# Optimization experiments

Hardware: AMD Instinct MI355X
Metric: run time of the kernel (lower is better)

The kernel has to match this reference:

```python
import jax, jax.numpy as jnp
import numpy as np

Q_DIM = 1024
K_DIM = 1024
V_DIM = 1024
ATTEN_DIM = 1024
NUM_HEADS = 16
HEAD_DIM = ATTEN_DIM // NUM_HEADS
B, L = 4, 2048


def setup_inputs() -> dict:
    key = jax.random.key(0)
    ks = jax.random.split(key, 11)
    s = 0.02
    return {
        "query": jax.random.normal(ks[0], (B, L, Q_DIM), dtype=jnp.float32),
        "key":   jax.random.normal(ks[1], (B, L, K_DIM), dtype=jnp.float32),
        "value": jax.random.normal(ks[2], (B, L, V_DIM), dtype=jnp.float32),
        "Wq": jax.random.normal(ks[3], (Q_DIM, ATTEN_DIM), dtype=jnp.float32) * s,
        "bq": jnp.zeros((ATTEN_DIM,), dtype=jnp.float32),
        "Wk": jax.random.normal(ks[4], (K_DIM, ATTEN_DIM), dtype=jnp.float32) * s,
        "bk": jnp.zeros((ATTEN_DIM,), dtype=jnp.float32),
        "Wv": jax.random.normal(ks[5], (V_DIM, ATTEN_DIM), dtype=jnp.float32) * s,
        "bv": jnp.zeros((ATTEN_DIM,), dtype=jnp.float32),
        "Wo": jax.random.normal(ks[6], (ATTEN_DIM, V_DIM), dtype=jnp.float32) * s,
        "bo": jnp.zeros((V_DIM,), dtype=jnp.float32),
    }


def reference(query, key, value, Wq, bq, Wk, bk, Wv, bv, Wo, bo):
    # QKV projections
    q = query @ Wq + bq        # [B, L, A]
    k = key   @ Wk + bk        # [B, L, A]
    v = value @ Wv + bv        # [B, L, A]
    # split heads: [B, L, H, D]
    def split_heads(x):
        return x.reshape(x.shape[:-1] + (NUM_HEADS, HEAD_DIM))
    q, k, v = split_heads(q), split_heads(k), split_heads(v)
    scale = 1.0 / (HEAD_DIM ** 0.5)
    # scores: [B, H, Lq, Lk]
    scores = jnp.einsum("bqhd,bkhd->bhqk", q, k) * scale
    attn = jax.nn.softmax(scores, axis=-1)
    out = jnp.einsum("bhqk,bkhd->bqhd", attn, v)  # [B, Lq, H, D]
    out = out.reshape(out.shape[0], out.shape[1], ATTEN_DIM)
    return out @ Wo + bo
```

## Files before the change

kernel.cpp:

```cpp
#include <hip/hip_runtime.h>
#include <stdint.h>

#define L_SEQ 2048
#define BATCH 4
#define ADIM  1024
#define NH    16
#define HD    64

typedef __attribute__((ext_vector_type(8))) short bf16x8;
typedef __attribute__((ext_vector_type(4))) float f32x4;
typedef __attribute__((ext_vector_type(16))) float f32x16;
typedef __attribute__((ext_vector_type(2))) int i32x2;

__device__ __forceinline__ short f2bf(float f) {
    union { float f; unsigned u; } x; x.f = f;
    unsigned r = x.u + 0x7fffu + ((x.u >> 16) & 1u);
    return (short)(r >> 16);
}

__device__ __forceinline__ void async_ld16(void* lds, const void* g) {
    __builtin_amdgcn_global_load_lds(
        (const __attribute__((address_space(1))) void*)g,
        (__attribute__((address_space(3))) void*)lds, 16, 0, 0);
}

__device__ __forceinline__ int cvtpk_bf16(float a, float b) {
    int r;
    asm("v_cvt_pk_bf16_f32 %0, %1, %2" : "=v"(r) : "v"(a), "v"(b));
    return r;
}

__device__ __forceinline__ bf16x8 pack4(int a, int b, int c, int d) {
    union { int i[4]; bf16x8 v; } u;
    u.i[0] = a; u.i[1] = b; u.i[2] = c; u.i[3] = d;
    return u.v;
}

__global__ void cvt3_kernel(const float* __restrict__ s0, const float* __restrict__ s1,
                            const float* __restrict__ s2, short* __restrict__ dst, int n4) {
    int i = blockIdx.x * blockDim.x + threadIdx.x;
    if (i >= n4) return;
    int z = blockIdx.y;
    const float* src = (z == 0) ? s0 : (z == 1) ? s1 : s2;
    float4 v = reinterpret_cast<const float4*>(src)[i];
    short4 s;
    s.x = f2bf(v.x); s.y = f2bf(v.y); s.z = f2bf(v.z); s.w = f2bf(v.w);
    reinterpret_cast<short4*>(dst + (size_t)z * (BATCH * L_SEQ * ADIM))[i] = s;
}

__global__ void transpose4_kernel(const float* __restrict__ W0, const float* __restrict__ W1,
                                  const float* __restrict__ W2, const float* __restrict__ W3,
                                  short* __restrict__ outb) {
    __shared__ float t[32][33];
    int z = blockIdx.z;
    const float* in = (z == 0) ? W0 : (z == 1) ? W1 : (z == 2) ? W2 : W3;
    short* out = outb + (size_t)z * (ADIM * ADIM);
    int x  = blockIdx.x * 32 + threadIdx.x;
    int y0 = blockIdx.y * 32 + threadIdx.y;
#pragma unroll
    for (int j = 0; j < 4; ++j)
        t[threadIdx.y + 8 * j][threadIdx.x] = in[(y0 + 8 * j) * 1024 + x];
    __syncthreads();
    int x2 = blockIdx.y * 32 + threadIdx.x;
    int y2 = blockIdx.x * 32 + threadIdx.y;
#pragma unroll
    for (int j = 0; j < 4; ++j)
        out[(y2 + 8 * j) * 1024 + x2] = f2bf(t[threadIdx.x][threadIdx.y + 8 * j]);
}

__device__ __forceinline__ void gemm_core(const short* __restrict__ A,
                                          const short* __restrict__ BT,
                                          const float* __restrict__ bias,
                                          void* __restrict__ Cout,
                                          int mode, float scalemul,
                                          int m0, int n0) {
    const int K = 1024, N = 1024;
    __shared__ __align__(16) short smem[16384];
    int tid = threadIdx.x;
    int wave = tid >> 6, lane = tid & 63, quad = lane >> 4, l16 = lane & 15;
    int wm = wave & 1, wn = wave >> 1;
    f32x4 acc[4][4] = {};

    int row = tid >> 2, ck = tid & 3;
    const short* gA0 = A  + (size_t)(m0 + row) * K + ck * 8;
    const short* gA1 = gA0 + (size_t)64 * K;
    const short* gB0 = BT + (size_t)(n0 + row) * K + ck * 8;
    const short* gB1 = gB0 + (size_t)64 * K;
    int loA0 = tid * 8, loA1 = tid * 8 + 2048;
    int loB0 = tid * 8 + 4096, loB1 = tid * 8 + 6144;

    async_ld16(smem + loA0, gA0); async_ld16(smem + loA1, gA1);
    async_ld16(smem + loB0, gB0); async_ld16(smem + loB1, gB1);
    gA0 += 32; gA1 += 32; gB0 += 32; gB1 += 32;
    __syncthreads();

    int cur = 0;
    for (int t = 0; t < 32; ++t) {
        if (t < 31) {
            int off = (cur ^ 1) * 8192;
            async_ld16(smem + off + loA0, gA0); async_ld16(smem + off + loA1, gA1);
            async_ld16(smem + off + loB0, gB0); async_ld16(smem + off + loB1, gB1);
            gA0 += 32; gA1 += 32; gB0 += 32; gB1 += 32;
        }
        const short* Ab = smem + cur * 8192;
        const short* Bb = Ab + 4096;
        bf16x8 af[4], bfr[4];
#pragma unroll
        for (int mt = 0; mt < 4; ++mt)
            af[mt] = *(const bf16x8*)&Ab[(wm * 64 + mt * 16 + l16) * 32 + quad * 8];
#pragma unroll
        for (int nt = 0; nt < 4; ++nt)
            bfr[nt] = *(const bf16x8*)&Bb[(wn * 64 + nt * 16 + l16) * 32 + quad * 8];
#pragma unroll
        for (int mt = 0; mt < 4; ++mt)
#pragma unroll
            for (int nt = 0; nt < 4; ++nt)
                acc[mt][nt] = __builtin_amdgcn_mfma_f32_16x16x32_bf16(
                    af[mt], bfr[nt], acc[mt][nt], 0, 0, 0);
        __syncthreads();
        cur ^= 1;
    }

    if (mode == 0) {
#pragma unroll
        for (int nt = 0; nt < 4; ++nt) {
            int col = n0 + wn * 64 + nt * 16 + l16;
            float bv = bias[col];
#pragma unroll
            for (int mt = 0; mt < 4; ++mt)
#pragma unroll
                for (int r = 0; r < 4; ++r) {
                    int rw = m0 + wm * 64 + mt * 16 + quad * 4 + r;
                    ((short*)Cout)[(size_t)rw * N + col] = f2bf((acc[mt][nt][r] + bv) * scalemul);
                }
        }
    } else if (mode == 1) {
        short* tw = smem + wave * 1120;
        int rbase = m0 + wm * 64;
        int bidx = rbase >> 11, lk0 = rbase & 2047;
#pragma unroll
        for (int nt = 0; nt < 4; ++nt) {
            int col0 = n0 + wn * 64 + nt * 16;
            int h = col0 >> 6, d0 = col0 & 63;
            float bv = bias[col0 + l16];
#pragma unroll
            for (int mt = 0; mt < 4; ++mt) {
                int a0 = cvtpk_bf16(acc[mt][nt][0] + bv, acc[mt][nt][1] + bv);
                int a1 = cvtpk_bf16(acc[mt][nt][2] + bv, acc[mt][nt][3] + bv);
                *(int*)&tw[l16 * 70 + mt * 16 + quad * 4]     = a0;
                *(int*)&tw[l16 * 70 + mt * 16 + quad * 4 + 2] = a1;
            }
            int dl = lane >> 2;
            short* dst = (short*)Cout +
                (((size_t)bidx * NH + h) * HD + d0 + dl) * L_SEQ + lk0;
#pragma unroll
            for (int p = 0; p < 2; ++p) {
                int ch = (lane & 3) + p * 4;
                *(bf16x8*)&dst[ch * 8] = *(const bf16x8*)&tw[dl * 70 + ch * 8];
            }
        }
    } else {
#pragma unroll
        for (int nt = 0; nt < 4; ++nt) {
            int col = n0 + wn * 64 + nt * 16 + l16;
            float bv = bias[col];
#pragma unroll
            for (int mt = 0; mt < 4; ++mt)
#pragma unroll
                for (int r = 0; r < 4; ++r) {
                    int rw = m0 + wm * 64 + mt * 16 + quad * 4 + r;
                    ((float*)Cout)[(size_t)rw * N + col] = acc[mt][nt][r] + bv;
                }
        }
    }
}

__device__ __forceinline__ void gemm_swz(int& m0, int& n0) {
    int bid = blockIdx.y * 8 + blockIdx.x;
    int swz = (bid & 7) * 64 + (bid >> 3);
    n0 = (swz & 7) * 128;
    m0 = (swz >> 3) * 128;
}

__global__ __launch_bounds__(256, 4)
void gemm_one(const short* __restrict__ A, const short* __restrict__ BT,
              const float* __restrict__ bias, void* __restrict__ Cout,
              int mode, float scalemul) {
    int m0, n0; gemm_swz(m0, n0);
    gemm_core(A, BT, bias, Cout, mode, scalemul, m0, n0);
}

__global__ __launch_bounds__(256, 4)
void qkv_gemm(const short* __restrict__ Xbase, const short* __restrict__ WTbase,
              const float* __restrict__ bq, const float* __restrict__ bk,
              const float* __restrict__ bv,
              short* __restrict__ Qb, short* __restrict__ Kb, short* __restrict__ VTout,
              float qscale) {
    int z = blockIdx.z;
    const short* A  = Xbase + (size_t)z * (BATCH * L_SEQ * ADIM);
    const short* BT = WTbase + (size_t)z * (ADIM * ADIM);
    const float* bias = (z == 0) ? bq : (z == 1) ? bk : bv;
    void* out = (z == 0) ? (void*)Qb : (z == 1) ? (void*)Kb : (void*)VTout;
    int mode = (z == 2) ? 1 : 0;
    float sm = (z == 0) ? qscale : 1.0f;
    int m0, n0; gemm_swz(m0, n0);
    gemm_core(A, BT, bias, out, mode, sm, m0, n0);
}

__global__ __launch_bounds__(256, 4)
void attn_kernel(const short* __restrict__ Qb, const short* __restrict__ Kb,
                 const short* __restrict__ VT, short* __restrict__ Oout) {
    __shared__ __align__(16) short lds[16384];
    int tid = threadIdx.x;
    int wave = tid >> 6, lane = tid & 63;
    int r31 = lane & 31, hi = lane >> 5;

    int f = (blockIdx.z * NH + blockIdx.y) * (L_SEQ / 128) + blockIdx.x;
    int swz = (f & 7) * 128 + (f >> 3);
    int qb = swz & 15;
    int h  = (swz >> 4) & 15;
    int b  = swz >> 8;

    size_t qrow = (size_t)(b * L_SEQ + qb * 128 + wave * 32 + r31) * ADIM + h * HD;
    bf16x8 qf[4];
#pragma unroll
    for (int dc = 0; dc < 4; ++dc)
        qf[dc] = *(const bf16x8*)&Qb[qrow + dc * 16 + hi * 8];

    const short* Kbase = Kb + (size_t)b * L_SEQ * ADIM + h * HD;
    const short* Vbase = VT + ((size_t)(b * NH + h) * HD) * L_SEQ;
    const short* gp[4]; int step[4]; int ldso[4];
#pragma unroll
    for (int s = 0; s < 4; ++s) {
        int j = s * 256 + tid;
        ldso[s] = j * 8;
        if (j < 512) {
            int c = j >> 6, k = j & 63;
            gp[s] = Kbase + (size_t)k * ADIM + c * 8;
            step[s] = 64 * ADIM;
        } else {
            int jv = j - 512;
            int c = jv >> 6, d = jv & 63;
            gp[s] = Vbase + (size_t)d * L_SEQ + c * 8;
            step[s] = 64;
        }
    }

    f32x16 o0 = {}, o1 = {}, lacc = {};
    const bf16x8 ones = pack4(0x3F803F80, 0x3F803F80, 0x3F803F80, 0x3F803F80);

#pragma unroll
    for (int s = 0; s < 4; ++s) { async_ld16(lds + ldso[s], gp[s]); gp[s] += step[s]; }
    __syncthreads();

    int cur = 0;
    for (int t = 0; t < 32; ++t) {
        const short* kb_l = lds + cur * 8192;
        const short* vb_l = kb_l + 4096;
        if (t < 31) {
            short* dst = lds + (cur ^ 1) * 8192;
#pragma unroll
            for (int s = 0; s < 4; ++s) { async_ld16(dst + ldso[s], gp[s]); gp[s] += step[s]; }
        }
#pragma unroll
        for (int kt = 0; kt < 2; ++kt) {
            f32x16 sv = {};
            __builtin_amdgcn_s_setprio(1);
#pragma unroll
            for (int dc = 0; dc < 4; ++dc) {
                bf16x8 kf = *(const bf16x8*)&kb_l[(((dc << 1) + hi) * 64 + kt * 32 + r31) * 8];
                sv = __builtin_amdgcn_mfma_f32_32x32x16_bf16(kf, qf[dc], sv, 0, 0, 0);
            }
            __builtin_amdgcn_s_setprio(0);
#pragma unroll
            for (int r = 0; r < 16; ++r) sv[r] = __builtin_amdgcn_exp2f(sv[r]);

            int p0 = cvtpk_bf16(sv[0],  sv[1]);
            int p1 = cvtpk_bf16(sv[2],  sv[3]);
            int p2 = cvtpk_bf16(sv[4],  sv[5]);
            int p3 = cvtpk_bf16(sv[6],  sv[7]);
            int p4 = cvtpk_bf16(sv[8],  sv[9]);
            int p5 = cvtpk_bf16(sv[10], sv[11]);
            int p6 = cvtpk_bf16(sv[12], sv[13]);
            int p7 = cvtpk_bf16(sv[14], sv[15]);
            asm volatile("v_permlane32_swap_b32 %0, %1" : "+v"(p0), "+v"(p2));
            asm volatile("v_permlane32_swap_b32 %0, %1" : "+v"(p1), "+v"(p3));
            asm volatile("v_permlane32_swap_b32 %0, %1" : "+v"(p4), "+v"(p6));
            asm volatile("v_permlane32_swap_b32 %0, %1" : "+v"(p5), "+v"(p7));
            bf16x8 pf0 = pack4(p0, p1, p2, p3);
            bf16x8 pf1 = pack4(p4, p5, p6, p7);

            bf16x8 vf00 = *(const bf16x8*)&vb_l[((kt * 4 + hi)     * 64 + r31) * 8];
            bf16x8 vf01 = *(const bf16x8*)&vb_l[((kt * 4 + 2 + hi) * 64 + r31) * 8];
            bf16x8 vf10 = *(const bf16x8*)&vb_l[((kt * 4 + hi)     * 64 + 32 + r31) * 8];
            bf16x8 vf11 = *(const bf16x8*)&vb_l[((kt * 4 + 2 + hi) * 64 + 32 + r31) * 8];
            __builtin_amdgcn_s_setprio(1);
            o0 = __builtin_amdgcn_mfma_f32_32x32x16_bf16(vf00, pf0, o0, 0, 0, 0);
            o1 = __builtin_amdgcn_mfma_f32_32x32x16_bf16(vf10, pf0, o1, 0, 0, 0);
            lacc = __builtin_amdgcn_mfma_f32_32x32x16_bf16(ones, pf0, lacc, 0, 0, 0);
            o0 = __builtin_amdgcn_mfma_f32_32x32x16_bf16(vf01, pf1, o0, 0, 0, 0);
            o1 = __builtin_amdgcn_mfma_f32_32x32x16_bf16(vf11, pf1, o1, 0, 0, 0);
            lacc = __builtin_amdgcn_mfma_f32_32x32x16_bf16(ones, pf1, lacc, 0, 0, 0);
            __builtin_amdgcn_s_setprio(0);
        }
        __syncthreads();
        cur ^= 1;
    }

    float inv = __builtin_amdgcn_rcpf(lacc[0]);

    short* tile = lds + wave * (32 * 68);
#pragma unroll
    for (int dt = 0; dt < 2; ++dt)
#pragma unroll
        for (int g = 0; g < 4; ++g) {
            int d0 = dt * 32 + g * 8 + hi * 4;
            int pa, pb;
            if (dt == 0) {
                pa = cvtpk_bf16(o0[g * 4 + 0] * inv, o0[g * 4 + 1] * inv);
                pb = cvtpk_bf16(o0[g * 4 + 2] * inv, o0[g * 4 + 3] * inv);
            } else {
                pa = cvtpk_bf16(o1[g * 4 + 0] * inv, o1[g * 4 + 1] * inv);
                pb = cvtpk_bf16(o1[g * 4 + 2] * inv, o1[g * 4 + 3] * inv);
            }
            *(i32x2*)&tile[r31 * 68 + d0] = (i32x2){pa, pb};
        }
    __syncthreads();
    size_t obase = (size_t)(b * L_SEQ + qb * 128 + wave * 32) * ADIM + h * HD;
    int rr = lane >> 3, cc = lane & 7;
#pragma unroll
    for (int p = 0; p < 4; ++p) {
        int row = p * 8 + rr;
        bf16x8 v = *(const bf16x8*)&tile[row * 68 + cc * 8];
        *(bf16x8*)&Oout[obase + (size_t)row * ADIM + cc * 8] = v;
    }
}

extern "C" void kernel_launch(void* const* d_in, const int* in_sizes, int n_in,
                              void* d_out, int out_size, void* d_ws, size_t ws_size,
                              hipStream_t stream) {
    const float* query = (const float*)d_in[0];
    const float* keyp  = (const float*)d_in[1];
    const float* value = (const float*)d_in[2];
    const float* Wq = (const float*)d_in[3];
    const float* bq = (const float*)d_in[4];
    const float* Wk = (const float*)d_in[5];
    const float* bk = (const float*)d_in[6];
    const float* Wv = (const float*)d_in[7];
    const float* bv = (const float*)d_in[8];
    const float* Wo = (const float*)d_in[9];
    const float* bo = (const float*)d_in[10];

    const float QSCALE = 0.125f * 1.44269504f;
    const size_t MB = 1ull << 20;
    const int n4 = (BATCH * L_SEQ * ADIM) / 4;
    char* w = (char*)d_ws;
    dim3 tblk(32, 8);
    dim3 gemm_grid(ADIM / 128, (BATCH * L_SEQ) / 128);
    dim3 attn_grid(L_SEQ / 128, NH, BATCH);

    if (ws_size >= 104 * MB) {
        short* X0  = (short*)(w);
        short* WT  = (short*)(w + 48 * MB);
        short* VT  = (short*)(w + 56 * MB);
        short* Kb  = (short*)(w + 72 * MB);
        short* Qb  = (short*)(w + 88 * MB);
        short* AO  = X0;

        cvt3_kernel<<<dim3(n4 / 256, 3), 256, 0, stream>>>(query, keyp, value, X0, n4);
        transpose4_kernel<<<dim3(32, 32, 4), tblk, 0, stream>>>(Wq, Wk, Wv, Wo, WT);
        qkv_gemm<<<dim3(ADIM / 128, (BATCH * L_SEQ) / 128, 3), 256, 0, stream>>>(
            X0, WT, bq, bk, bv, Qb, Kb, VT, QSCALE);
        attn_kernel<<<attn_grid, 256, 0, stream>>>(Qb, Kb, VT, AO);
        gemm_one<<<gemm_grid, 256, 0, stream>>>(AO, WT + (size_t)3 * ADIM * ADIM, bo,
                                                d_out, 2, 1.0f);
    } else {
        short* X0  = (short*)(w);
        short* WT  = (short*)(w + 16 * MB);
        short* VT  = (short*)(w + 24 * MB);
        short* Kb  = (short*)(w + 40 * MB);
        short* Qb  = (short*)(w + 56 * MB);

        transpose4_kernel<<<dim3(32, 32, 4), tblk, 0, stream>>>(Wq, Wk, Wv, Wo, WT);
        cvt3_kernel<<<dim3(n4 / 256, 1), 256, 0, stream>>>(query, query, query, X0, n4);
        gemm_one<<<gemm_grid, 256, 0, stream>>>(X0, WT, bq, Qb, 0, QSCALE);
        cvt3_kernel<<<dim3(n4 / 256, 1), 256, 0, stream>>>(keyp, keyp, keyp, X0, n4);
        gemm_one<<<gemm_grid, 256, 0, stream>>>(X0, WT + (size_t)ADIM * ADIM, bk, Kb, 0, 1.0f);
        cvt3_kernel<<<dim3(n4 / 256, 1), 256, 0, stream>>>(value, value, value, X0, n4);
        gemm_one<<<gemm_grid, 256, 0, stream>>>(X0, WT + (size_t)2 * ADIM * ADIM, bv, VT, 1, 1.0f);
        attn_kernel<<<attn_grid, 256, 0, stream>>>(Qb, Kb, VT, X0);
        gemm_one<<<gemm_grid, 256, 0, stream>>>(X0, WT + (size_t)3 * ADIM * ADIM, bo,
                                                d_out, 2, 1.0f);
    }
}
```

Baseline: 335.2 us.

## Fuse fp32-to-bf16 input conversion into QKV GEMM A-tile loads

Drops the separate cvt3 pass that turned the query, key and value activations into bf16 in workspace. A new GEMM core async-loads fp32 A tiles straight into LDS with an XOR swizzle and converts them to bf16 at fragment-load time, just before the MFMAs. This avoids writing and re-reading 48MB of bf16 activations. In exchange the A tile in LDS doubles in size, LDS use grows to 48KB and occupancy drops to 3 blocks. The conversion work is now repeated by every N-tile block, 8 times per A tile, and the small-workspace branch is removed.

Measured after the change: 352.0 us. 5.0% more time.

```diff
diff --git a/kernel.cpp b/kernel.cpp
--- a/kernel.cpp
+++ b/kernel.cpp
@@ -34,18 +34,6 @@
     union { int i[4]; bf16x8 v; } u;
     u.i[0] = a; u.i[1] = b; u.i[2] = c; u.i[3] = d;
     return u.v;
-}
-
-__global__ void cvt3_kernel(const float* __restrict__ s0, const float* __restrict__ s1,
-                            const float* __restrict__ s2, short* __restrict__ dst, int n4) {
-    int i = blockIdx.x * blockDim.x + threadIdx.x;
-    if (i >= n4) return;
-    int z = blockIdx.y;
-    const float* src = (z == 0) ? s0 : (z == 1) ? s1 : s2;
-    float4 v = reinterpret_cast<const float4*>(src)[i];
-    short4 s;
-    s.x = f2bf(v.x); s.y = f2bf(v.y); s.z = f2bf(v.z); s.w = f2bf(v.w);
-    reinterpret_cast<short4*>(dst + (size_t)z * (BATCH * L_SEQ * ADIM))[i] = s;
 }
 
 __global__ void transpose4_kernel(const float* __restrict__ W0, const float* __restrict__ W1,
@@ -66,6 +54,13 @@
 #pragma unroll
     for (int j = 0; j < 4; ++j)
         out[(y2 + 8 * j) * 1024 + x2] = f2bf(t[threadIdx.x][threadIdx.y + 8 * j]);
+}
+
+__device__ __forceinline__ void gemm_swz(int& m0, int& n0) {
+    int bid = blockIdx.y * 8 + blockIdx.x;
+    int swz = (bid & 7) * 64 + (bid >> 3);
+    n0 = (swz & 7) * 128;
+    m0 = (swz >> 3) * 128;
 }
 
 __device__ __forceinline__ void gemm_core(const short* __restrict__ A,
@@ -134,7 +129,113 @@
                     ((short*)Cout)[(size_t)rw * N + col] = f2bf((acc[mt][nt][r] + bv) * scalemul);
                 }
         }
-    } else if (mode == 1) {
+    } else {
+#pragma unroll
+        for (int nt = 0; nt < 4; ++nt) {
+            int col = n0 + wn * 64 + nt * 16 + l16;
+            float bv = bias[col];
+#pragma unroll
+            for (int mt = 0; mt < 4; ++mt)
+#pragma unroll
+                for (int r = 0; r < 4; ++r) {
+                    int rw = m0 + wm * 64 + mt * 16 + quad * 4 + r;
+                    ((float*)Cout)[(size_t)rw * N + col] = acc[mt][nt][r] + bv;
+                }
+        }
+    }
+}
+
+__global__ __launch_bounds__(256, 4)
+void gemm_one(const short* __restrict__ A, const short* __restrict__ BT,
+              const float* __restrict__ bias, void* __restrict__ Cout,
+              int mode, float scalemul) {
+    int m0, n0; gemm_swz(m0, n0);
+    gemm_core(A, BT, bias, Cout, mode, scalemul, m0, n0);
+}
+
+__device__ __forceinline__ void gemmf32_core(const float* __restrict__ A,
+                                             const short* __restrict__ BT,
+                                             const float* __restrict__ bias,
+                                             void* __restrict__ Cout,
+                                             int mode, float scalemul,
+                                             int m0, int n0) {
+    const int K = 1024, N = 1024;
+    __shared__ __align__(16) short smem[24576];
+    int tid = threadIdx.x;
+    int wave = tid >> 6, lane = tid & 63, quad = lane >> 4, l16 = lane & 15;
+    int wm = wave & 1, wn = wave >> 1;
+    f32x4 acc[4][4] = {};
+
+    const float* gA[4]; int loA[4];
+#pragma unroll
+    for (int s = 0; s < 4; ++s) {
+        int j = s * 256 + tid;
+        int row = j >> 3, c = (j & 7) ^ (row & 7);
+        gA[s] = A + (size_t)(m0 + row) * K + c * 4;
+        loA[s] = j * 8;
+    }
+    const short* gB[2]; int loB[2];
+#pragma unroll
+    for (int s = 0; s < 2; ++s) {
+        int j = s * 256 + tid;
+        int row = j >> 2, ck = j & 3;
+        gB[s] = BT + (size_t)(n0 + row) * K + ck * 8;
+        loB[s] = 8192 + j * 8;
+    }
+
+#pragma unroll
+    for (int s = 0; s < 4; ++s) { async_ld16(smem + loA[s], gA[s]); gA[s] += 32; }
+#pragma unroll
+    for (int s = 0; s < 2; ++s) { async_ld16(smem + loB[s], gB[s]); gB[s] += 32; }
+    __syncthreads();
+
+    int cur = 0;
+    for (int t = 0; t < 32; ++t) {
+        if (t < 31) {
+            int off = (cur ^ 1) * 12288;
+#pragma unroll
+            for (int s = 0; s < 4; ++s) { async_ld16(smem + off + loA[s], gA[s]); gA[s] += 32; }
+#pragma unroll
+            for (int s = 0; s < 2; ++s) { async_ld16(smem + off + loB[s], gB[s]); gB[s] += 32; }
+        }
+        const short* Ab = smem + cur * 12288;
+        const short* Bb = Ab + 8192;
+        bf16x8 af[4], bfr[4];
+#pragma unroll
+        for (int mt = 0; mt < 4; ++mt) {
+            int r = wm * 64 + mt * 16 + l16;
+            float4 f0 = *(const float4*)&Ab[(r * 8 + ((2 * quad)     ^ (r & 7))) * 8];
+            float4 f1 = *(const float4*)&Ab[(r * 8 + ((2 * quad + 1) ^ (r & 7))) * 8];
+            af[mt] = pack4(cvtpk_bf16(f0.x, f0.y), cvtpk_bf16(f0.z, f0.w),
+                           cvtpk_bf16(f1.x, f1.y), cvtpk_bf16(f1.z, f1.w));
+        }
+#pragma unroll
+        for (int nt = 0; nt < 4; ++nt)
+            bfr[nt] = *(const bf16x8*)&Bb[(wn * 64 + nt * 16 + l16) * 32 + quad * 8];
+#pragma unroll
+        for (int mt = 0; mt < 4; ++mt)
+#pragma unroll
+            for (int nt = 0; nt < 4; ++nt)
+                acc[mt][nt] = __builtin_amdgcn_mfma_f32_16x16x32_bf16(
+                    af[mt], bfr[nt], acc[mt][nt], 0, 0, 0);
+        __syncthreads();
+        cur ^= 1;
+    }
+
+    if (mode == 0) {
+#pragma unroll
+        for (int nt = 0; nt < 4; ++nt) {
+            int col = n0 + wn * 64 + nt * 16 + l16;
+            float bv = bias[col];
+#pragma unroll
+            for (int mt = 0; mt < 4; ++mt)
+#pragma unroll
+                for (int r = 0; r < 4; ++r) {
+                    int rw = m0 + wm * 64 + mt * 16 + quad * 4 + r;
+                    ((short*)Cout)[(size_t)rw * N + col] = f2bf((acc[mt][nt][r] + bv) * scalemul);
+                }
+        }
+    } else {
         short* tw = smem + wave * 1120;
         int rbase = m0 + wm * 64;
         int bidx = rbase >> 11, lk0 = rbase & 2047;
@@ -159,52 +260,25 @@
                 *(bf16x8*)&dst[ch * 8] = *(const bf16x8*)&tw[dl * 70 + ch * 8];
             }
         }
-    } else {
-#pragma unroll
-        for (int nt = 0; nt < 4; ++nt) {
-            int col = n0 + wn * 64 + nt * 16 + l16;
-            float bv = bias[col];
-#pragma unroll
-            for (int mt = 0; mt < 4; ++mt)
-#pragma unroll
-                for (int r = 0; r < 4; ++r) {
-                    int rw = m0 + wm * 64 + mt * 16 + quad * 4 + r;
-                    ((float*)Cout)[(size_t)rw * N + col] = acc[mt][nt][r] + bv;
-                }
-        }
-    }
-}
-
-__device__ __forceinline__ void gemm_swz(int& m0, int& n0) {
-    int bid = blockIdx.y * 8 + blockIdx.x;
-    int swz = (bid & 7) * 64 + (bid >> 3);
-    n0 = (swz & 7) * 128;
-    m0 = (swz >> 3) * 128;
-}
-
-__global__ __launch_bounds__(256, 4)
-void gemm_one(const short* __restrict__ A, const short* __restrict__ BT,
-              const float* __restrict__ bias, void* __restrict__ Cout,
-              int mode, float scalemul) {
-    int m0, n0; gemm_swz(m0, n0);
-    gemm_core(A, BT, bias, Cout, mode, scalemul, m0, n0);
-}
-
-__global__ __launch_bounds__(256, 4)
-void qkv_gemm(const short* __restrict__ Xbase, const short* __restrict__ WTbase,
+    }
+}
+
+__global__ __launch_bounds__(256, 3)
+void qkv_gemm(const float* __restrict__ Xq, const float* __restrict__ Xk,
+              const float* __restrict__ Xv, const short* __restrict__ WTbase,
               const float* __restrict__ bq, const float* __restrict__ bk,
               const float* __restrict__ bv,
               short* __restrict__ Qb, short* __restrict__ Kb, short* __restrict__ VTout,
               float qscale) {
     int z = blockIdx.z;
-    const short* A  = Xbase + (size_t)z * (BATCH * L_SEQ * ADIM);
+    const float* A = (z == 0) ? Xq : (z == 1) ? Xk : Xv;
     const short* BT = WTbase + (size_t)z * (ADIM * ADIM);
     const float* bias = (z == 0) ? bq : (z == 1) ? bk : bv;
     void* out = (z == 0) ? (void*)Qb : (z == 1) ? (void*)Kb : (void*)VTout;
     int mode = (z == 2) ? 1 : 0;
     float sm = (z == 0) ? qscale : 1.0f;
     int m0, n0; gemm_swz(m0, n0);
-    gemm_core(A, BT, bias, out, mode, sm, m0, n0);
+    gemmf32_core(A, BT, bias, out, mode, sm, m0, n0);
 }
 
 __global__ __launch_bounds__(256, 4)
@@ -353,43 +427,21 @@
 
     const float QSCALE = 0.125f * 1.44269504f;
     const size_t MB = 1ull << 20;
-    const int n4 = (BATCH * L_SEQ * ADIM) / 4;
     char* w = (char*)d_ws;
     dim3 tblk(32, 8);
     dim3 gemm_grid(ADIM / 128, (BATCH * L_SEQ) / 128);
     dim3 attn_grid(L_SEQ / 128, NH, BATCH);
 
-    if (ws_size >= 104 * MB) {
-        short* X0  = (short*)(w);
-        short* WT  = (short*)(w + 48 * MB);
-        short* VT  = (short*)(w + 56 * MB);
-        short* Kb  = (short*)(w + 72 * MB);
-        short* Qb  = (short*)(w + 88 * MB);
-        short* AO  = X0;
-
-        cvt3_kernel<<<dim3(n4 / 256, 3), 256, 0, stream>>>(query, keyp, value, X0, n4);
-        transpose4_kernel<<<dim3(32, 32, 4), tblk, 0, stream>>>(Wq, Wk, Wv, Wo, WT);
-        qkv_gemm<<<dim3(ADIM / 128, (BATCH * L_SEQ) / 128, 3), 256, 0, stream>>>(
-            X0, WT, bq, bk, bv, Qb, Kb, VT, QSCALE);
-        attn_kernel<<<attn_grid, 256, 0, stream>>>(Qb, Kb, VT, AO);
-        gemm_one<<<gemm_grid, 256, 0, stream>>>(AO, WT + (size_t)3 * ADIM * ADIM, bo,
-                                                d_out, 2, 1.0f);
-    } else {
-        short* X0  = (short*)(w);
-        short* WT  = (short*)(w + 16 * MB);
-        short* VT  = (short*)(w + 24 * MB);
-        short* Kb  = (short*)(w + 40 * MB);
-        short* Qb  = (short*)(w + 56 * MB);
-
-        transpose4_kernel<<<dim3(32, 32, 4), tblk, 0, stream>>>(Wq, Wk, Wv, Wo, WT);
-        cvt3_kernel<<<dim3(n4 / 256, 1), 256, 0, stream>>>(query, query, query, X0, n4);
-        gemm_one<<<gemm_grid, 256, 0, stream>>>(X0, WT, bq, Qb, 0, QSCALE);
-        cvt3_kernel<<<dim3(n4 / 256, 1), 256, 0, stream>>>(keyp, keyp, keyp, X0, n4);
-        gemm_one<<<gemm_grid, 256, 0, stream>>>(X0, WT + (size_t)ADIM * ADIM, bk, Kb, 0, 1.0f);
-        cvt3_kernel<<<dim3(n4 / 256, 1), 256, 0, stream>>>(value, value, value, X0, n4);
-        gemm_one<<<gemm_grid, 256, 0, stream>>>(X0, WT + (size_t)2 * ADIM * ADIM, bv, VT, 1, 1.0f);
-        attn_kernel<<<attn_grid, 256, 0, stream>>>(Qb, Kb, VT, X0);
-        gemm_one<<<gemm_grid, 256, 0, stream>>>(X0, WT + (size_t)3 * ADIM * ADIM, bo,
-                                                d_out, 2, 1.0f);
-    }
-}
+    short* AO = (short*)(w);
+    short* WT = (short*)(w + 16 * MB);
+    short* VT = (short*)(w + 24 * MB);
+    short* Kb = (short*)(w + 40 * MB);
+    short* Qb = (short*)(w + 56 * MB);
+
+    transpose4_kernel<<<dim3(32, 32, 4), tblk, 0, stream>>>(Wq, Wk, Wv, Wo, WT);
+    qkv_gemm<<<dim3(ADIM / 128, (BATCH * L_SEQ) / 128, 3), 256, 0, stream>>>(
+        query, keyp, value, WT, bq, bk, bv, Qb, Kb, VT, QSCALE);
+    attn_kernel<<<attn_grid, 256, 0, stream>>>(Qb, Kb, VT, AO);
+    gemm_one<<<gemm_grid, 256, 0, stream>>>(AO, WT + (size_t)3 * ADIM * ADIM, bo,
+                                            d_out, 2, 1.0f);
+}
```

## Rework GEMM into 8-wave 128x256 tiles with 4-stage ping-pong pipeline

Applied to the files above, without the earlier changes.

The projection GEMM core goes from 256-thread 128x128 tiles with a double buffer to 512-thread blocks on 128x256 tiles. It adds a four-stage LDS ring loaded asynchronously, with explicit vmcnt waits and raw s_barrier calls. MFMA work is split into half-steps interleaved with staged loads, and s_setprio raises priority during the MFMA bursts. The goal is to hide global-load latency and cut per-tile sync and reload overhead. The cost is 96KB of LDS per block, which limits occupancy, and fragile hand-tuned waitcnt ordering.

Result: no change. 330.0 us (-1.6%).

```diff
diff --git a/kernel.cpp b/kernel.cpp
--- a/kernel.cpp
+++ b/kernel.cpp
@@ -68,58 +68,100 @@
         out[(y2 + 8 * j) * 1024 + x2] = f2bf(t[threadIdx.x][threadIdx.y + 8 * j]);
 }
 
-__device__ __forceinline__ void gemm_core(const short* __restrict__ A,
-                                          const short* __restrict__ BT,
-                                          const float* __restrict__ bias,
-                                          void* __restrict__ Cout,
-                                          int mode, float scalemul,
-                                          int m0, int n0) {
+
+#define GBAR() asm volatile("s_barrier" ::: "memory")
+
+#define GP_PAIR(HB, SHB, DOSTAGE, NWAIT)                                          \
+  {                                                                               \
+    const short* Ah = smem + (HB) * 12288;                                        \
+    const short* Bh = Ah + 4096;                                                  \
+    if (DOSTAGE) {                                                                \
+      async_ld16(smem + (SHB) * 12288 + loA,  pA);                                \
+      async_ld16(smem + (SHB) * 12288 + loB0, pB0);                               \
+    }                                                                             \
+    bf16x8 b0 = *(const bf16x8*)&Bh[(wn * 64 +  0 + l16) * 32 + quad * 8];        \
+    bf16x8 b1 = *(const bf16x8*)&Bh[(wn * 64 + 16 + l16) * 32 + quad * 8];        \
+    bf16x8 b2 = *(const bf16x8*)&Bh[(wn * 64 + 32 + l16) * 32 + quad * 8];        \
+    bf16x8 b3 = *(const bf16x8*)&Bh[(wn * 64 + 48 + l16) * 32 + quad * 8];        \
+    bf16x8 a0 = *(const bf16x8*)&Ah[(wm * 64 +  0 + l16) * 32 + quad * 8];        \
+    bf16x8 a1 = *(const bf16x8*)&Ah[(wm * 64 + 16 + l16) * 32 + quad * 8];        \
+    GBAR();                                                                       \
+    __builtin_amdgcn_s_setprio(1);                                                \
+    acc[0][0] = __builtin_amdgcn_mfma_f32_16x16x32_bf16(a0, b0, acc[0][0], 0,0,0);\
+    acc[0][1] = __builtin_amdgcn_mfma_f32_16x16x32_bf16(a0, b1, acc[0][1], 0,0,0);\
+    acc[0][2] = __builtin_amdgcn_mfma_f32_16x16x32_bf16(a0, b2, acc[0][2], 0,0,0);\
+    acc[0][3] = __builtin_amdgcn_mfma_f32_16x16x32_bf16(a0, b3, acc[0][3], 0,0,0);\
+    acc[1][0] = __builtin_amdgcn_mfma_f32_16x16x32_bf16(a1, b0, acc[1][0], 0,0,0);\
+    acc[1][1] = __builtin_amdgcn_mfma_f32_16x16x32_bf16(a1, b1, acc[1][1], 0,0,0);\
+    acc[1][2] = __builtin_amdgcn_mfma_f32_16x16x32_bf16(a1, b2, acc[1][2], 0,0,0);\
+    acc[1][3] = __builtin_amdgcn_mfma_f32_16x16x32_bf16(a1, b3, acc[1][3], 0,0,0);\
+    __builtin_amdgcn_s_setprio(0);                                                \
+    GBAR();                                                                       \
+    if (DOSTAGE) {                                                                \
+      async_ld16(smem + (SHB) * 12288 + loB1, pB1);                               \
+      pA += 32; pB0 += 32; pB1 += 32;                                             \
+    }                                                                             \
+    bf16x8 a2 = *(const bf16x8*)&Ah[(wm * 64 + 32 + l16) * 32 + quad * 8];        \
+    bf16x8 a3 = *(const bf16x8*)&Ah[(wm * 64 + 48 + l16) * 32 + quad * 8];        \
+    GBAR();                                                                       \
+    __builtin_amdgcn_s_setprio(1);                                                \
+    acc[2][0] = __builtin_amdgcn_mfma_f32_16x16x32_bf16(a2, b0, acc[2][0], 0,0,0);\
+    acc[2][1] = __builtin_amdgcn_mfma_f32_16x16x32_bf16(a2, b1, acc[2][1], 0,0,0);\
+    acc[2][2] = __builtin_amdgcn_mfma_f32_16x16x32_bf16(a2, b2, acc[2][2], 0,0,0);\
+    acc[2][3] = __builtin_amdgcn_mfma_f32_16x16x32_bf16(a2, b3, acc[2][3], 0,0,0);\
+    acc[3][0] = __builtin_amdgcn_mfma_f32_16x16x32_bf16(a3, b0, acc[3][0], 0,0,0);\
+    acc[3][1] = __builtin_amdgcn_mfma_f32_16x16x32_bf16(a3, b1, acc[3][1], 0,0,0);\
+    acc[3][2] = __builtin_amdgcn_mfma_f32_16x16x32_bf16(a3, b2, acc[3][2], 0,0,0);\
+    acc[3][3] = __builtin_amdgcn_mfma_f32_16x16x32_bf16(a3, b3, acc[3][3], 0,0,0);\
+    __builtin_amdgcn_s_setprio(0);                                                \
+    if ((NWAIT) == 6)      asm volatile("s_waitcnt vmcnt(6)" ::: "memory");       \
+    else if ((NWAIT) == 3) asm volatile("s_waitcnt vmcnt(3)" ::: "memory");       \
+    else if ((NWAIT) == 0) asm volatile("s_waitcnt vmcnt(0)" ::: "memory");       \
+    __builtin_amdgcn_sched_barrier(0);                                            \
+    GBAR();                                                                       \
+  }
+
+__device__ __forceinline__ void gemm8p_core(const short* __restrict__ A,
+                                            const short* __restrict__ BT,
+                                            const float* __restrict__ bias,
+                                            void* __restrict__ Cout,
+                                            int mode, float scalemul,
+                                            int m0, int n0) {
     const int K = 1024, N = 1024;
-    __shared__ __align__(16) short smem[16384];
+    __shared__ __align__(16) short smem[49152];
     int tid = threadIdx.x;
     int wave = tid >> 6, lane = tid & 63, quad = lane >> 4, l16 = lane & 15;
-    int wm = wave & 1, wn = wave >> 1;
+    int wm = wave >> 2, wn = wave & 3;
     f32x4 acc[4][4] = {};
 
-    int row = tid >> 2, ck = tid & 3;
-    const short* gA0 = A  + (size_t)(m0 + row) * K + ck * 8;
-    const short* gA1 = gA0 + (size_t)64 * K;
-    const short* gB0 = BT + (size_t)(n0 + row) * K + ck * 8;
-    const short* gB1 = gB0 + (size_t)64 * K;
-    int loA0 = tid * 8, loA1 = tid * 8 + 2048;
-    int loB0 = tid * 8 + 4096, loB1 = tid * 8 + 6144;
-
-    async_ld16(smem + loA0, gA0); async_ld16(smem + loA1, gA1);
-    async_ld16(smem + loB0, gB0); async_ld16(smem + loB1, gB1);
-    gA0 += 32; gA1 += 32; gB0 += 32; gB1 += 32;
+    int row4 = tid >> 2, kq = tid & 3;
+    const short* pA  = A  + (size_t)(m0 + row4) * K + kq * 8;
+    const short* pB0 = BT + (size_t)(n0 + row4) * K + kq * 8;
+    const short* pB1 = BT + (size_t)(n0 + 128 + row4) * K + kq * 8;
+    int loA = tid * 8, loB0 = 4096 + tid * 8, loB1 = 8192 + tid * 8;
+
+#pragma unroll
+    for (int h = 0; h < 3; ++h) {
+        async_ld16(smem + h * 12288 + loA,  pA);
+        async_ld16(smem + h * 12288 + loB0, pB0);
+        async_ld16(smem + h * 12288 + loB1, pB1);
+        pA += 32; pB0 += 32; pB1 += 32;
+    }
+    asm volatile("s_waitcnt vmcnt(6)" ::: "memory");
+    __builtin_amdgcn_sched_barrier(0);
+    GBAR();
+
+    for (int tt = 0; tt < 7; ++tt) {
+        GP_PAIR(0, 3, true, 6)
+        GP_PAIR(1, 0, true, 6)
+        GP_PAIR(2, 1, true, 6)
+        GP_PAIR(3, 2, true, 6)
+    }
+    GP_PAIR(0, 3, true,  6)
+    GP_PAIR(1, 0, false, 3)
+    GP_PAIR(2, 1, false, 0)
+    GP_PAIR(3, 2, false, -1)
     __syncthreads();
-
-    int cur = 0;
-    for (int t = 0; t < 32; ++t) {
-        if (t < 31) {
-            int off = (cur ^ 1) * 8192;
-            async_ld16(smem + off + loA0, gA0); async_ld16(smem + off + loA1, gA1);
-            async_ld16(smem + off + loB0, gB0); async_ld16(smem + off + loB1, gB1);
-            gA0 += 32; gA1 += 32; gB0 += 32; gB1 += 32;
-        }
-        const short* Ab = smem + cur * 8192;
-        const short* Bb = Ab + 4096;
-        bf16x8 af[4], bfr[4];
-#pragma unroll
-        for (int mt = 0; mt < 4; ++mt)
-            af[mt] = *(const bf16x8*)&Ab[(wm * 64 + mt * 16 + l16) * 32 + quad * 8];
-#pragma unroll
-        for (int nt = 0; nt < 4; ++nt)
-            bfr[nt] = *(const bf16x8*)&Bb[(wn * 64 + nt * 16 + l16) * 32 + quad * 8];
-#pragma unroll
-        for (int mt = 0; mt < 4; ++mt)
-#pragma unroll
-            for (int nt = 0; nt < 4; ++nt)
-                acc[mt][nt] = __builtin_amdgcn_mfma_f32_16x16x32_bf16(
-                    af[mt], bfr[nt], acc[mt][nt], 0, 0, 0);
-        __syncthreads();
-        cur ^= 1;
-    }
 
     if (mode == 0) {
 #pragma unroll
@@ -175,22 +217,22 @@
     }
 }
 
-__device__ __forceinline__ void gemm_swz(int& m0, int& n0) {
-    int bid = blockIdx.y * 8 + blockIdx.x;
-    int swz = (bid & 7) * 64 + (bid >> 3);
-    n0 = (swz & 7) * 128;
-    m0 = (swz >> 3) * 128;
-}
-
-__global__ __launch_bounds__(256, 4)
+__device__ __forceinline__ void gemm8p_swz(int& m0, int& n0) {
+    int bid = blockIdx.y * 4 + blockIdx.x;
+    int swz = (bid & 7) * 32 + (bid >> 3);
+    n0 = (swz & 3) * 256;
+    m0 = (swz >> 2) * 128;
+}
+
+__global__ __launch_bounds__(512, 2)
 void gemm_one(const short* __restrict__ A, const short* __restrict__ BT,
               const float* __restrict__ bias, void* __restrict__ Cout,
               int mode, float scalemul) {
-    int m0, n0; gemm_swz(m0, n0);
-    gemm_core(A, BT, bias, Cout, mode, scalemul, m0, n0);
-}
-
-__global__ __launch_bounds__(256, 4)
+    int m0, n0; gemm8p_swz(m0, n0);
+    gemm8p_core(A, BT, bias, Cout, mode, scalemul, m0, n0);
+}
+
+__global__ __launch_bounds__(512, 2)
 void qkv_gemm(const short* __restrict__ Xbase, const short* __restrict__ WTbase,
               const float* __restrict__ bq, const float* __restrict__ bk,
               const float* __restrict__ bv,
@@ -203,8 +245,8 @@
     void* out = (z == 0) ? (void*)Qb : (z == 1) ? (void*)Kb : (void*)VTout;
     int mode = (z == 2) ? 1 : 0;
     float sm = (z == 0) ? qscale : 1.0f;
-    int m0, n0; gemm_swz(m0, n0);
-    gemm_core(A, BT, bias, out, mode, sm, m0, n0);
+    int m0, n0; gemm8p_swz(m0, n0);
+    gemm8p_core(A, BT, bias, out, mode, sm, m0, n0);
 }
 
 __global__ __launch_bounds__(256, 4)
@@ -356,7 +398,7 @@
     const int n4 = (BATCH * L_SEQ * ADIM) / 4;
     char* w = (char*)d_ws;
     dim3 tblk(32, 8);
-    dim3 gemm_grid(ADIM / 128, (BATCH * L_SEQ) / 128);
+    dim3 gemm_grid(ADIM / 256, (BATCH * L_SEQ) / 128);
     dim3 attn_grid(L_SEQ / 128, NH, BATCH);
 
     if (ws_size >= 104 * MB) {
@@ -369,10 +411,10 @@
 
         cvt3_kernel<<<dim3(n4 / 256, 3), 256, 0, stream>>>(query, keyp, value, X0, n4);
         transpose4_kernel<<<dim3(32, 32, 4), tblk, 0, stream>>>(Wq, Wk, Wv, Wo, WT);
-        qkv_gemm<<<dim3(ADIM / 128, (BATCH * L_SEQ) / 128, 3), 256, 0, stream>>>(
+        qkv_gemm<<<dim3(ADIM / 256, (BATCH * L_SEQ) / 128, 3), 512, 0, stream>>>(
             X0, WT, bq, bk, bv, Qb, Kb, VT, QSCALE);
         attn_kernel<<<attn_grid, 256, 0, stream>>>(Qb, Kb, VT, AO);
-        gemm_one<<<gemm_grid, 256, 0, stream>>>(AO, WT + (size_t)3 * ADIM * ADIM, bo,
+        gemm_one<<<gemm_grid, 512, 0, stream>>>(AO, WT + (size_t)3 * ADIM * ADIM, bo,
                                                 d_out, 2, 1.0f);
     } else {
         short* X0  = (short*)(w);
@@ -383,13 +425,13 @@
 
         transpose4_kernel<<<dim3(32, 32, 4), tblk, 0, stream>>>(Wq, Wk, Wv, Wo, WT);
         cvt3_kernel<<<dim3(n4 / 256, 1), 256, 0, stream>>>(query, query, query, X0, n4);
-        gemm_one<<<gemm_grid, 256, 0, stream>>>(X0, WT, bq, Qb, 0, QSCALE);
+        gemm_one<<<gemm_grid, 512, 0, stream>>>(X0, WT, bq, Qb, 0, QSCALE);
         cvt3_kernel<<<dim3(n4 / 256, 1), 256, 0, stream>>>(keyp, keyp, keyp, X0, n4);
-        gemm_one<<<gemm_grid, 256, 0, stream>>>(X0, WT + (size_t)ADIM * ADIM, bk, Kb, 0, 1.0f);
+        gemm_one<<<gemm_grid, 512, 0, stream>>>(X0, WT + (size_t)ADIM * ADIM, bk, Kb, 0, 1.0f);
         cvt3_kernel<<<dim3(n4 / 256, 1), 256, 0, stream>>>(value, value, value, X0, n4);
-        gemm_one<<<gemm_grid, 256, 0, stream>>>(X0, WT + (size_t)2 * ADIM * ADIM, bv, VT, 1, 1.0f);
+        gemm_one<<<gemm_grid, 512, 0, stream>>>(X0, WT + (size_t)2 * ADIM * ADIM, bv, VT, 1, 1.0f);
         attn_kernel<<<attn_grid, 256, 0, stream>>>(Qb, Kb, VT, X0);
-        gemm_one<<<gemm_grid, 256, 0, stream>>>(X0, WT + (size_t)3 * ADIM * ADIM, bo,
+        gemm_one<<<gemm_grid, 512, 0, stream>>>(X0, WT + (size_t)3 * ADIM * ADIM, bo,
                                                 d_out, 2, 1.0f);
     }
 }
```
